# Kernel optimization log

Hardware: AMD Instinct MI355X
Metric: run time of the kernel (lower is better)

Reference implementation:

```python
import jax, jax.numpy as jnp
import numpy as np

MAX_DIST = 32  # unidirectional T5-style bucketing: num_buckets = 33
N_HEAD, D_K, D_V = 8, 64, 64


def setup_inputs() -> dict:
    key = jax.random.key(0)
    ks = jax.random.split(key, 9)
    B, S, D = 4, 2048, 512
    q = jax.random.normal(ks[0], (B, S, D), dtype=jnp.float32)
    k = jax.random.normal(ks[1], (B, S, D), dtype=jnp.float32)
    v = jax.random.normal(ks[2], (B, S, D), dtype=jnp.float32)
    mask = jax.random.randint(ks[3], (B, 1, 1, S), 0, 2, dtype=jnp.int32)
    sc = 1.0 / np.sqrt(D)
    Wq = jax.random.normal(ks[4], (D, D), dtype=jnp.float32) * sc
    Wk = jax.random.normal(ks[5], (D, D), dtype=jnp.float32) * sc
    Wv = jax.random.normal(ks[6], (D, D), dtype=jnp.float32) * sc
    Wfc = jax.random.normal(ks[7], (D, D), dtype=jnp.float32) * sc
    rel_bias = jax.random.normal(ks[8], (MAX_DIST + 1, N_HEAD), dtype=jnp.float32)
    return {"q": q, "k": k, "v": v, "mask": mask, "Wq": Wq, "Wk": Wk,
            "Wv": Wv, "Wfc": Wfc, "rel_bias": rel_bias}


def _rel_pos_bias(rel_bias, seq_len):
    # unidirectional: bucket = clamp(max(context - memory, 0), 0, MAX_DIST)
    pos = jnp.arange(seq_len)
    n = pos[:, None] - pos[None, :]              # context - memory = -relative_position
    bucket = jnp.clip(jnp.maximum(n, 0), 0, MAX_DIST)
    vals = rel_bias[bucket]                      # (S, S, H)
    return jnp.transpose(vals, (2, 0, 1))[None]  # (1, H, S, S)


def reference(q, k, v, mask, Wq, Wk, Wv, Wfc, rel_bias):
    B, Sq, _ = q.shape
    Sk = k.shape[1]
    scale = D_K ** (-0.5)
    qh = (q @ Wq).reshape(B, Sq, N_HEAD, D_K).transpose(0, 2, 1, 3)  # bhsd
    kh = (k @ Wk).reshape(B, Sk, N_HEAD, D_K).transpose(0, 2, 1, 3)
    vh = (v @ Wv).reshape(B, Sk, N_HEAD, D_V).transpose(0, 2, 1, 3)
    attn = jnp.einsum('bhqd,bhkd->bhqk', qh, kh) * scale
    attn = attn + _rel_pos_bias(rel_bias, Sq)
    attn = jnp.where(mask == 0, jnp.float32(-1e9), attn)
    attn = jax.nn.softmax(attn, axis=-1)          # dropout is identity at eval
    out = jnp.einsum('bhqk,bhkd->bhqd', attn, vh)
    out = out.transpose(0, 2, 1, 3).reshape(B, Sq, N_HEAD * D_V)
    out = out @ Wfc
    return out, attn
```

## Files before the change

### kernel.cpp

```cpp
#include <hip/hip_runtime.h>


typedef __attribute__((ext_vector_type(8))) short bfrag;
typedef __attribute__((ext_vector_type(4))) short s16x4;
typedef __attribute__((ext_vector_type(4))) float f32x4;
typedef unsigned int u32;

#define MFMA16(a,b,c) __builtin_amdgcn_mfma_f32_16x16x32_bf16(a,b,c,0,0,0)

__device__ __forceinline__ void gl_lds16(const void* g, void* l){
  __builtin_amdgcn_global_load_lds((const __attribute__((address_space(1))) u32*)g,
                                   (__attribute__((address_space(3))) u32*)l, 16, 0, 0);
}
__device__ __forceinline__ short f2bs(float f){
  u32 u = __float_as_uint(f);
  u = (u + 0x7fffu + ((u>>16)&1u)) >> 16;
  return (short)u;
}
__device__ __forceinline__ float b2f(short s){
  return __uint_as_float(((u32)(unsigned short)s) << 16);
}

#define BB 4
#define HH 8
#define SS 2048
#define DD 512

#define WQT_OFF  0u
#define WKT_OFF  524288u
#define WVT_OFF  1048576u
#define WFCT_OFF 1572864u
#define QB_OFF   2097152u
#define KB_OFF   10485760u
#define VB_OFF   18874368u
#define QH_OFF   27262976u
#define KH_OFF   35651584u
#define VT_OFF   44040192u
#define OH_OFF   52428800u

__global__ __launch_bounds__(256) void conv_w_k(const float* w0,const float* w1,
                                                const float* w2,const float* w3, char* ws){
  const float* w; short* o;
  switch(blockIdx.z){
    case 0:  w=w0; o=(short*)(ws+WQT_OFF); break;
    case 1:  w=w1; o=(short*)(ws+WKT_OFF); break;
    case 2:  w=w2; o=(short*)(ws+WVT_OFF); break;
    default: w=w3; o=(short*)(ws+WFCT_OFF); break;
  }
  int t  = blockIdx.x*256 + threadIdx.x;
  int n  = t >> 6;
  int k0 = (t & 63) << 3;
  bfrag v;
  #pragma unroll
  for (int j=0;j<8;++j) v[j] = f2bs(w[(k0+j)*512 + n]);
  *(bfrag*)(o + n*512 + k0) = v;
}

__global__ __launch_bounds__(256) void conv_x_k(const float* x0,const float* x1,
                                                const float* x2, char* ws){
  const float* x; short* o;
  switch(blockIdx.z){
    case 0:  x=x0; o=(short*)(ws+QB_OFF); break;
    case 1:  x=x1; o=(short*)(ws+KB_OFF); break;
    default: x=x2; o=(short*)(ws+VB_OFF); break;
  }
  int i = (blockIdx.x*256 + threadIdx.x) << 3;
  float4 a = *(const float4*)(x+i);
  float4 b = *(const float4*)(x+i+4);
  bfrag v;
  v[0]=f2bs(a.x); v[1]=f2bs(a.y); v[2]=f2bs(a.z); v[3]=f2bs(a.w);
  v[4]=f2bs(b.x); v[5]=f2bs(b.y); v[6]=f2bs(b.z); v[7]=f2bs(b.w);
  *(bfrag*)(o+i) = v;
}

__device__ void gemm_core(const short* A, const short* Bt, char* Cout, int mode, int bid){
  __shared__ __align__(16) char lds[32768];
  int i0, j0;
  if (mode==1){ i0 = (bid&3)<<7; j0 = (bid>>2)<<7; }
  else        { i0 = (bid>>2)<<7; j0 = (bid&3)<<7; }
  int tid = threadIdx.x;
  int l = tid & 63, w = tid >> 6;
  int wr = (w>>1)<<6, wc = (w&1)<<6;
  int l15 = l & 15, l4 = l >> 4;
  f32x4 acc[4][4];
  #pragma unroll
  for(int a=0;a<4;++a)
    #pragma unroll
    for(int b=0;b<4;++b) acc[a][b] = (f32x4){0.f,0.f,0.f,0.f};
  const char* Ab = (const char*)A;
  const char* Bb = (const char*)Bt;
  for (int kk=0; kk<8; ++kk){
    #pragma unroll
    for (int it=0; it<4; ++it){
      int ci = it*256 + tid;
      int row = ci>>3, cc = ci&7;
      gl_lds16(Ab + (size_t)(i0+row)*1024 + kk*128 + ((cc^(row&7))<<4),
               lds + ((it*256 + w*64)<<4));
      gl_lds16(Bb + (size_t)(j0+row)*1024 + kk*128 + ((cc^(row&7))<<4),
               lds + 16384 + ((it*256 + w*64)<<4));
    }
    asm volatile("s_waitcnt vmcnt(0)" ::: "memory");
    __syncthreads();
    #pragma unroll
    for (int kb=0; kb<2; ++kb){
      bfrag af[4], bf[4];
      #pragma unroll
      for (int mi=0;mi<4;++mi){
        int row = wr + mi*16 + l15;
        af[mi] = *(const bfrag*)(lds + row*128 + (((kb*4 + l4) ^ (row&7))<<4));
      }
      #pragma unroll
      for (int ni=0;ni<4;++ni){
        int row = wc + ni*16 + l15;
        bf[ni] = *(const bfrag*)(lds + 16384 + row*128 + (((kb*4 + l4) ^ (row&7))<<4));
      }
      #pragma unroll
      for (int mi=0;mi<4;++mi)
        #pragma unroll
        for (int ni=0;ni<4;++ni)
          acc[mi][ni] = MFMA16(af[mi], bf[ni], acc[mi][ni]);
    }
    __syncthreads();
  }
  #pragma unroll
  for (int mi=0;mi<4;++mi){
    #pragma unroll
    for (int ni=0;ni<4;++ni){
      #pragma unroll
      for (int r=0;r<4;++r){
        int i = i0 + wr + mi*16 + (l4<<2) + r;
        int j = j0 + wc + ni*16 + l15;
        float v = acc[mi][ni][r];
        if (mode==2){
          ((float*)Cout)[(size_t)i*512 + j] = v;
        } else if (mode==0){
          size_t o = ((size_t)(((i>>11)<<3) + (j>>6))*2048 + (size_t)(i&2047))*64 + (j&63);
          ((short*)Cout)[o] = f2bs(v);
        } else {
          size_t o = ((size_t)(((j>>11)<<3) + (i>>6))*64 + (size_t)(i&63))*2048 + (j&2047);
          ((short*)Cout)[o] = f2bs(v);
        }
      }
    }
  }
}

__global__ __launch_bounds__(256,2) void gemm_proj_k(char* ws){
  switch(blockIdx.z){
    case 0:  gemm_core((const short*)(ws+QB_OFF),  (const short*)(ws+WQT_OFF), ws+QH_OFF, 0, blockIdx.x); break;
    case 1:  gemm_core((const short*)(ws+KB_OFF),  (const short*)(ws+WKT_OFF), ws+KH_OFF, 0, blockIdx.x); break;
    default: gemm_core((const short*)(ws+WVT_OFF), (const short*)(ws+VB_OFF),  ws+VT_OFF, 1, blockIdx.x); break;
  }
}
__global__ __launch_bounds__(256,2) void gemm_final_k(char* ws, float* out){
  gemm_core((const short*)(ws+OH_OFF), (const short*)(ws+WFCT_OFF), (char*)out, 2, blockIdx.x);
}

#define MSK_OFF_L   65536
#define BIAS_OFF_L  73728
#define WSUM_OFF_L  73872
#define RECIP_OFF_L 74384
#define PVRED_OFF_L 74448
#define LDS_TOTAL   78592

__global__ __launch_bounds__(512,1) void attn_k(char* ws, const int* mask,
                                                const float* rel_bias, float* attn_out){
  extern __shared__ __align__(16) char sm[];
  int tid = threadIdx.x;
  int l = tid & 63, w = tid >> 6;
  int l15 = l & 15, l4 = l >> 4;
  int bh = blockIdx.x, qblk = blockIdx.y;
  int b = bh >> 3, h = bh & 7;
  const short* qhb = (const short*)(ws+QH_OFF) + (size_t)bh*SS*64;
  const char*  khb = ws + KH_OFF + (size_t)bh*SS*128;
  const char*  vtb = ws + VT_OFF + (size_t)bh*64*SS*2;

  {
    const int4* m4 = (const int4*)(mask + b*SS);
    int4 ma = m4[tid];
    float4* mf = (float4*)(sm + MSK_OFF_L);
    mf[tid] = make_float4(ma.x?1.f:0.f, ma.y?1.f:0.f, ma.z?1.f:0.f, ma.w?1.f:0.f);
  }
  if (tid < 33) ((float*)(sm+BIAS_OFF_L))[tid] = rel_bias[tid*HH + h];

  int qrow = (qblk<<4) + l15;
  bfrag qA0 = *(const bfrag*)(qhb + (size_t)qrow*64 + l4*8);
  bfrag qA1 = *(const bfrag*)(qhb + (size_t)qrow*64 + 32 + l4*8);
  const float* biasl = (const float*)(sm+BIAS_OFF_L);
  const float* maskl = (const float*)(sm+MSK_OFF_L);
  float rsum[4] = {0.f,0.f,0.f,0.f};

  __syncthreads();

  int wbase = w << 8;
  #pragma unroll 2
  for (int t=0; t<16; ++t){
    int rowk = wbase + (t<<4) + l15;
    const char* kr = khb + (size_t)rowk*128 + (l4<<4);
    bfrag b0 = *(const bfrag*)(kr);
    bfrag b1 = *(const bfrag*)(kr + 64);
    f32x4 acc = (f32x4){0.f,0.f,0.f,0.f};
    acc = MFMA16(qA0, b0, acc);
    acc = MFMA16(qA1, b1, acc);
    float mval = maskl[rowk];
    int rl0 = l4<<2;
    int byte = rowk<<1;
    #pragma unroll
    for (int r=0;r<4;++r){
      int rowl = rl0 + r;
      int n = (qblk<<4) + rowl - rowk;
      n = n<0 ? 0 : (n>32 ? 32 : n);
      float s = acc[r]*0.125f + biasl[n];
      float p = mval * __expf(s);
      rsum[r] += p;
      int ch = (byte>>4) ^ rowl;
      *(short*)(sm + rowl*4096 + (ch<<4) + (byte&15)) = f2bs(p);
    }
  }

  {
    float* wsum = (float*)(sm+WSUM_OFF_L);
    #pragma unroll
    for (int r=0;r<4;++r){
      float s = rsum[r];
      s += __shfl_xor(s,1); s += __shfl_xor(s,2);
      s += __shfl_xor(s,4); s += __shfl_xor(s,8);
      if (l15==0) wsum[(w<<4) + (l4<<2) + r] = s;
    }
  }
  __syncthreads();
  if (tid < 16){
    float* wsum = (float*)(sm+WSUM_OFF_L);
    float t = 0.f;
    #pragma unroll
    for (int i=0;i<8;++i) t += wsum[(i<<4) + tid];
    ((float*)(sm+RECIP_OFF_L))[tid] = 1.f/t;
  }
  __syncthreads();
  const float* recip = (const float*)(sm+RECIP_OFF_L);

  f32x4 acco = (f32x4){0.f,0.f,0.f,0.f};
  int dbase = (w&3)<<4;
  int khalf = w>>2;
  int chbase = khalf<<7;
  const char* vr = vtb + (size_t)(dbase + l15)*4096 + (khalf<<11) + (l4<<4);
  #pragma unroll 4
  for (int vc=0; vc<32; ++vc){
    int ch = (chbase + (vc<<2) + l4) ^ l15;
    bfrag af = *(const bfrag*)(sm + l15*4096 + (ch<<4));
    bfrag bv = *(const bfrag*)(vr + (vc<<6));
    acco = MFMA16(af, bv, acco);
  }
  {
    f32x4* pvred = (f32x4*)(sm+PVRED_OFF_L);
    if (w >= 4) pvred[((w-4)<<6) + l] = acco;
    __syncthreads();
    if (w < 4){
      acco += pvred[(w<<6) + l];
      short* oh = (short*)(ws + OH_OFF);
      #pragma unroll
      for (int r=0;r<4;++r){
        int rowl = (l4<<2) + r;
        float rc = recip[rowl];
        size_t sg = (size_t)b*SS + (qblk<<4) + rowl;
        oh[sg*512 + h*64 + dbase + l15] = f2bs(acco[r]*rc);
      }
    }
  }

  {
    float* dst0 = attn_out + (size_t)bh*SS*SS + (size_t)(qblk<<4)*SS;
    #pragma unroll
    for (int rr=0; rr<2; ++rr){
      int rowl = (w<<1) + rr;
      float rc = recip[rowl];
      float* dst = dst0 + (size_t)rowl*SS;
      #pragma unroll
      for (int it=0; it<8; ++it){
        int col  = it*256 + (l<<2);
        int byte = col<<1;
        int ch = (byte>>4) ^ rowl;
        s16x4 pv = *(const s16x4*)(sm + rowl*4096 + (ch<<4) + (byte&15));
        f32x4 o = (f32x4){b2f(pv[0])*rc, b2f(pv[1])*rc, b2f(pv[2])*rc, b2f(pv[3])*rc};
        __builtin_nontemporal_store(o, (f32x4*)(dst+col));
      }
    }
  }
}

extern "C" void kernel_launch(void* const* d_in, const int* in_sizes, int n_in,
                              void* d_out, int out_size, void* d_ws, size_t ws_size,
                              hipStream_t stream){
  const float* q   = (const float*)d_in[0];
  const float* k   = (const float*)d_in[1];
  const float* v   = (const float*)d_in[2];
  const int*  mask = (const int*)  d_in[3];
  const float* Wq  = (const float*)d_in[4];
  const float* Wk  = (const float*)d_in[5];
  const float* Wv  = (const float*)d_in[6];
  const float* Wfc = (const float*)d_in[7];
  const float* rb  = (const float*)d_in[8];
  char* ws = (char*)d_ws;
  float* out  = (float*)d_out;
  float* attn = out + (size_t)BB*SS*512;

  (void)hipFuncSetAttribute((const void*)attn_k,
        hipFuncAttributeMaxDynamicSharedMemorySize, LDS_TOTAL);

  conv_w_k<<<dim3(128,1,4), 256, 0, stream>>>(Wq, Wk, Wv, Wfc, ws);
  conv_x_k<<<dim3(2048,1,3), 256, 0, stream>>>(q, k, v, ws);
  gemm_proj_k<<<dim3(256,1,3), 256, 0, stream>>>(ws);
  attn_k<<<dim3(32,128), 512, LDS_TOTAL, stream>>>(ws, mask, rb, attn);
  gemm_final_k<<<dim3(256,1,1), 256, 0, stream>>>(ws, out);
}
```

Baseline: 331.7 us.

## Make attention kernel persistent with double-buffered P tiles to overlap attn stores

The attention kernel now launches 256 persistent blocks, each handling 16 consecutive query tiles of one head. It double-buffers the bf16 probability tile in LDS so the previous tile's fp32 attention-matrix stores run interleaved with the next tile's QK^T and softmax work. The per-block mask and bias setup is amortized across tiles, and bias lookup is skipped for key chunks entirely outside the clamp window. LDS use roughly doubles and the kernel adds more barriers, which limits occupancy to one block per CU.

```diff
diff --git a/kernel.cpp b/kernel.cpp
--- a/kernel.cpp
+++ b/kernel.cpp
@@ -7,6 +7,9 @@
 typedef unsigned int u32;
 
 #define MFMA16(a,b,c) __builtin_amdgcn_mfma_f32_16x16x32_bf16(a,b,c,0,0,0)
+
+#define BAR() do{ asm volatile("s_waitcnt lgkmcnt(0)" ::: "memory"); \
+                  __builtin_amdgcn_s_barrier(); }while(0)
 
 __device__ __forceinline__ void gl_lds16(const void* g, void* l){
   __builtin_amdgcn_global_load_lds((const __attribute__((address_space(1))) u32*)g,
@@ -156,12 +159,14 @@
   gemm_core((const short*)(ws+OH_OFF), (const short*)(ws+WFCT_OFF), (char*)out, 2, blockIdx.x);
 }
 
-#define MSK_OFF_L   65536
-#define BIAS_OFF_L  73728
-#define WSUM_OFF_L  73872
-#define RECIP_OFF_L 74384
-#define PVRED_OFF_L 74448
-#define LDS_TOTAL   78592
+#define P0_OFF      0
+#define P1_OFF      65536
+#define MSK_OFF_L   131072
+#define BIAS_OFF_L  139264
+#define WSUM_OFF_L  139424
+#define RECIP_OFF_L 139968
+#define PVRED_OFF_L 140032
+#define LDS_TOTAL   144128
 
 __global__ __launch_bounds__(512,1) void attn_k(char* ws, const int* mask,
                                                 const float* rel_bias, float* attn_out){
@@ -169,11 +174,13 @@
   int tid = threadIdx.x;
   int l = tid & 63, w = tid >> 6;
   int l15 = l & 15, l4 = l >> 4;
-  int bh = blockIdx.x, qblk = blockIdx.y;
+  int j = blockIdx.x;
+  int bh = j & 31, qc = j >> 5;
   int b = bh >> 3, h = bh & 7;
   const short* qhb = (const short*)(ws+QH_OFF) + (size_t)bh*SS*64;
   const char*  khb = ws + KH_OFF + (size_t)bh*SS*128;
   const char*  vtb = ws + VT_OFF + (size_t)bh*64*SS*2;
+  float* attb = attn_out + (size_t)bh*SS*SS;
 
   {
     const int4* m4 = (const int4*)(mask + b*SS);
@@ -182,108 +189,144 @@
     mf[tid] = make_float4(ma.x?1.f:0.f, ma.y?1.f:0.f, ma.z?1.f:0.f, ma.w?1.f:0.f);
   }
   if (tid < 33) ((float*)(sm+BIAS_OFF_L))[tid] = rel_bias[tid*HH + h];
-
-  int qrow = (qblk<<4) + l15;
-  bfrag qA0 = *(const bfrag*)(qhb + (size_t)qrow*64 + l4*8);
-  bfrag qA1 = *(const bfrag*)(qhb + (size_t)qrow*64 + 32 + l4*8);
+  float bias0  = rel_bias[h];
+  float bias32 = rel_bias[32*HH + h];
   const float* biasl = (const float*)(sm+BIAS_OFF_L);
   const float* maskl = (const float*)(sm+MSK_OFF_L);
-  float rsum[4] = {0.f,0.f,0.f,0.f};
-
-  __syncthreads();
-
-  int wbase = w << 8;
-  #pragma unroll 2
-  for (int t=0; t<16; ++t){
-    int rowk = wbase + (t<<4) + l15;
-    const char* kr = khb + (size_t)rowk*128 + (l4<<4);
-    bfrag b0 = *(const bfrag*)(kr);
-    bfrag b1 = *(const bfrag*)(kr + 64);
-    f32x4 acc = (f32x4){0.f,0.f,0.f,0.f};
-    acc = MFMA16(qA0, b0, acc);
-    acc = MFMA16(qA1, b1, acc);
-    float mval = maskl[rowk];
-    int rl0 = l4<<2;
-    int byte = rowk<<1;
-    #pragma unroll
-    for (int r=0;r<4;++r){
-      int rowl = rl0 + r;
-      int n = (qblk<<4) + rowl - rowk;
-      n = n<0 ? 0 : (n>32 ? 32 : n);
-      float s = acc[r]*0.125f + biasl[n];
-      float p = mval * __expf(s);
-      rsum[r] += p;
-      int ch = (byte>>4) ^ rowl;
-      *(short*)(sm + rowl*4096 + (ch<<4) + (byte&15)) = f2bs(p);
-    }
-  }
-
-  {
-    float* wsum = (float*)(sm+WSUM_OFF_L);
-    #pragma unroll
-    for (int r=0;r<4;++r){
-      float s = rsum[r];
-      s += __shfl_xor(s,1); s += __shfl_xor(s,2);
-      s += __shfl_xor(s,4); s += __shfl_xor(s,8);
-      if (l15==0) wsum[(w<<4) + (l4<<2) + r] = s;
-    }
-  }
-  __syncthreads();
-  if (tid < 16){
-    float* wsum = (float*)(sm+WSUM_OFF_L);
-    float t = 0.f;
-    #pragma unroll
-    for (int i=0;i<8;++i) t += wsum[(i<<4) + tid];
-    ((float*)(sm+RECIP_OFF_L))[tid] = 1.f/t;
-  }
-  __syncthreads();
   const float* recip = (const float*)(sm+RECIP_OFF_L);
-
-  f32x4 acco = (f32x4){0.f,0.f,0.f,0.f};
-  int dbase = (w&3)<<4;
-  int khalf = w>>2;
-  int chbase = khalf<<7;
-  const char* vr = vtb + (size_t)(dbase + l15)*4096 + (khalf<<11) + (l4<<4);
-  #pragma unroll 4
-  for (int vc=0; vc<32; ++vc){
-    int ch = (chbase + (vc<<2) + l4) ^ l15;
-    bfrag af = *(const bfrag*)(sm + l15*4096 + (ch<<4));
-    bfrag bv = *(const bfrag*)(vr + (vc<<6));
-    acco = MFMA16(af, bv, acco);
-  }
-  {
-    f32x4* pvred = (f32x4*)(sm+PVRED_OFF_L);
-    if (w >= 4) pvred[((w-4)<<6) + l] = acco;
-    __syncthreads();
-    if (w < 4){
-      acco += pvred[(w<<6) + l];
-      short* oh = (short*)(ws + OH_OFF);
-      #pragma unroll
-      for (int r=0;r<4;++r){
-        int rowl = (l4<<2) + r;
-        float rc = recip[rowl];
-        size_t sg = (size_t)b*SS + (qblk<<4) + rowl;
-        oh[sg*512 + h*64 + dbase + l15] = f2bs(acco[r]*rc);
-      }
-    }
-  }
-
-  {
-    float* dst0 = attn_out + (size_t)bh*SS*SS + (size_t)(qblk<<4)*SS;
-    #pragma unroll
-    for (int rr=0; rr<2; ++rr){
-      int rowl = (w<<1) + rr;
-      float rc = recip[rowl];
-      float* dst = dst0 + (size_t)rowl*SS;
-      #pragma unroll
-      for (int it=0; it<8; ++it){
-        int col  = it*256 + (l<<2);
+  int rl0 = l4<<2;
+  int qprev = 0;
+
+  for (int item=0; item<16; ++item){
+    int qblk = (qc<<4) + item;
+    char* pcur = sm + ((item&1) ? P1_OFF : P0_OFF);
+    const char* pprv = sm + ((item&1) ? P0_OFF : P1_OFF);
+
+    BAR();
+
+    float rcA = recip[(w<<1)];
+    float rcB = recip[(w<<1)+1];
+    float* dstp = attb + (size_t)(qprev<<4)*SS;
+
+    int qrow = (qblk<<4) + l15;
+    bfrag qA0 = *(const bfrag*)(qhb + (size_t)qrow*64 + l4*8);
+    bfrag qA1 = *(const bfrag*)(qhb + (size_t)qrow*64 + 32 + l4*8);
+    float rsum[4] = {0.f,0.f,0.f,0.f};
+    int r0 = qblk<<4;
+
+    #pragma unroll 2
+    for (int t=0; t<16; ++t){
+      int c0 = (w<<8) + (t<<4);
+      int rowk = c0 + l15;
+      const char* kr = khb + (size_t)rowk*128 + (l4<<4);
+      bfrag b0 = *(const bfrag*)(kr);
+      bfrag b1 = *(const bfrag*)(kr + 64);
+      if (item > 0){
+        int rowl = (w<<1) + (t>>3);
+        int col  = ((t&7)<<8) + (l<<2);
         int byte = col<<1;
         int ch = (byte>>4) ^ rowl;
-        s16x4 pv = *(const s16x4*)(sm + rowl*4096 + (ch<<4) + (byte&15));
+        s16x4 pv = *(const s16x4*)(pprv + rowl*4096 + (ch<<4) + (byte&15));
+        float rc = (t>>3) ? rcB : rcA;
         f32x4 o = (f32x4){b2f(pv[0])*rc, b2f(pv[1])*rc, b2f(pv[2])*rc, b2f(pv[3])*rc};
-        __builtin_nontemporal_store(o, (f32x4*)(dst+col));
-      }
+        __builtin_nontemporal_store(o, (f32x4*)(dstp + (size_t)rowl*SS + col));
+      }
+      f32x4 acc = (f32x4){0.f,0.f,0.f,0.f};
+      acc = MFMA16(qA0, b0, acc);
+      acc = MFMA16(qA1, b1, acc);
+      float mval = maskl[rowk];
+      float pr[4];
+      if (c0 >= r0+16){
+        #pragma unroll
+        for (int r=0;r<4;++r) pr[r] = __expf(acc[r]*0.125f + bias0);
+      } else if (c0 <= r0-47){
+        #pragma unroll
+        for (int r=0;r<4;++r) pr[r] = __expf(acc[r]*0.125f + bias32);
+      } else {
+        #pragma unroll
+        for (int r=0;r<4;++r){
+          int n = r0 + rl0 + r - rowk;
+          n = n<0 ? 0 : (n>32 ? 32 : n);
+          pr[r] = __expf(acc[r]*0.125f + biasl[n]);
+        }
+      }
+      int byte = rowk<<1;
+      #pragma unroll
+      for (int r=0;r<4;++r){
+        float p = mval * pr[r];
+        rsum[r] += p;
+        int rowl = rl0 + r;
+        int ch = (byte>>4) ^ rowl;
+        *(short*)(pcur + rowl*4096 + (ch<<4) + (byte&15)) = f2bs(p);
+      }
+    }
+
+    {
+      float* wsum = (float*)(sm+WSUM_OFF_L);
+      #pragma unroll
+      for (int r=0;r<4;++r){
+        float s = rsum[r];
+        s += __shfl_xor(s,1); s += __shfl_xor(s,2);
+        s += __shfl_xor(s,4); s += __shfl_xor(s,8);
+        if (l15==0) wsum[(w<<4) + rl0 + r] = s;
+      }
+    }
+    BAR();
+    if (tid < 16){
+      float* wsum = (float*)(sm+WSUM_OFF_L);
+      float t2 = 0.f;
+      #pragma unroll
+      for (int i=0;i<8;++i) t2 += wsum[(i<<4) + tid];
+      ((float*)(sm+RECIP_OFF_L))[tid] = 1.f/t2;
+    }
+    BAR();
+
+    f32x4 acco = (f32x4){0.f,0.f,0.f,0.f};
+    int dbase = (w&3)<<4;
+    int khalf = w>>2;
+    int chbase = khalf<<7;
+    const char* vr = vtb + (size_t)(dbase + l15)*4096 + (khalf<<11) + (l4<<4);
+    #pragma unroll 4
+    for (int vc=0; vc<32; ++vc){
+      int ch = (chbase + (vc<<2) + l4) ^ l15;
+      bfrag af = *(const bfrag*)(pcur + l15*4096 + (ch<<4));
+      bfrag bv = *(const bfrag*)(vr + (vc<<6));
+      acco = MFMA16(af, bv, acco);
+    }
+    {
+      f32x4* pvred = (f32x4*)(sm+PVRED_OFF_L);
+      if (w >= 4) pvred[((w-4)<<6) + l] = acco;
+      BAR();
+      if (w < 4){
+        acco += pvred[(w<<6) + l];
+        short* oh = (short*)(ws + OH_OFF);
+        #pragma unroll
+        for (int r=0;r<4;++r){
+          int rowl = rl0 + r;
+          float rc = recip[rowl];
+          size_t sg = (size_t)b*SS + (qblk<<4) + rowl;
+          oh[sg*512 + h*64 + dbase + l15] = f2bs(acco[r]*rc);
+        }
+      }
+    }
+    qprev = qblk;
+  }
+
+  {
+    const char* plast = sm + P1_OFF;
+    float* dstp = attb + (size_t)(qprev<<4)*SS;
+    float rcA = recip[(w<<1)];
+    float rcB = recip[(w<<1)+1];
+    #pragma unroll
+    for (int t=0; t<16; ++t){
+      int rowl = (w<<1) + (t>>3);
+      int col  = ((t&7)<<8) + (l<<2);
+      int byte = col<<1;
+      int ch = (byte>>4) ^ rowl;
+      s16x4 pv = *(const s16x4*)(plast + rowl*4096 + (ch<<4) + (byte&15));
+      float rc = (t>>3) ? rcB : rcA;
+      f32x4 o = (f32x4){b2f(pv[0])*rc, b2f(pv[1])*rc, b2f(pv[2])*rc, b2f(pv[3])*rc};
+      __builtin_nontemporal_store(o, (f32x4*)(dstp + (size_t)rowl*SS + col));
     }
   }
 }
@@ -310,6 +353,6 @@
   conv_w_k<<<dim3(128,1,4), 256, 0, stream>>>(Wq, Wk, Wv, Wfc, ws);
   conv_x_k<<<dim3(2048,1,3), 256, 0, stream>>>(q, k, v, ws);
   gemm_proj_k<<<dim3(256,1,3), 256, 0, stream>>>(ws);
-  attn_k<<<dim3(32,128), 512, LDS_TOTAL, stream>>>(ws, mask, rb, attn);
+  attn_k<<<dim3(256), 512, LDS_TOTAL, stream>>>(ws, mask, rb, attn);
   gemm_final_k<<<dim3(256,1,1), 256, 0, stream>>>(ws, out);
 }
```

Result: slower. 391.0 us (+17.9%).

## Recompute QK scores in fp32 for attn output and swap MFMA operand order

Applied to the files above, without the earlier changes.

The attention kernel swaps the MFMA A/B operands so each lane holds four consecutive key columns for one query row. That lets mask loads, bf16 packing and LDS stores become vector operations, and the row sum needs only two shuffles. Bias lookup is skipped for tiles entirely outside the bucketing window. The fp32 attention output is now written by recomputing QK^T and exp in a second pass and scaling by the reciprocal, instead of reading back bf16 probabilities from LDS. This trades extra MFMA, exp work and K reloads for higher precision and fewer LDS reads, and it also raises launch-bounds occupancy and replaces syncthreads with a custom barrier.

```diff
diff --git a/kernel.cpp b/kernel.cpp
--- a/kernel.cpp
+++ b/kernel.cpp
@@ -1,12 +1,15 @@
 #include <hip/hip_runtime.h>
+#include <hip/hip_bf16.h>
 
 
 typedef __attribute__((ext_vector_type(8))) short bfrag;
-typedef __attribute__((ext_vector_type(4))) short s16x4;
 typedef __attribute__((ext_vector_type(4))) float f32x4;
 typedef unsigned int u32;
 
 #define MFMA16(a,b,c) __builtin_amdgcn_mfma_f32_16x16x32_bf16(a,b,c,0,0,0)
+
+#define BAR() do{ asm volatile("s_waitcnt lgkmcnt(0)" ::: "memory"); \
+                  __builtin_amdgcn_s_barrier(); }while(0)
 
 __device__ __forceinline__ void gl_lds16(const void* g, void* l){
   __builtin_amdgcn_global_load_lds((const __attribute__((address_space(1))) u32*)g,
@@ -17,8 +20,10 @@
   u = (u + 0x7fffu + ((u>>16)&1u)) >> 16;
   return (short)u;
 }
-__device__ __forceinline__ float b2f(short s){
-  return __uint_as_float(((u32)(unsigned short)s) << 16);
+__device__ __forceinline__ u32 pack2(float a, float b){
+  float2 t; t.x = a; t.y = b;
+  __hip_bfloat162 h = __float22bfloat162_rn(t);
+  return *(u32*)&h;
 }
 
 #define BB 4
@@ -163,7 +168,7 @@
 #define PVRED_OFF_L 74448
 #define LDS_TOTAL   78592
 
-__global__ __launch_bounds__(512,1) void attn_k(char* ws, const int* mask,
+__global__ __launch_bounds__(512,4) void attn_k(char* ws, const int* mask,
                                                 const float* rel_bias, float* attn_out){
   extern __shared__ __align__(16) char sm[];
   int tid = threadIdx.x;
@@ -182,62 +187,104 @@
     mf[tid] = make_float4(ma.x?1.f:0.f, ma.y?1.f:0.f, ma.z?1.f:0.f, ma.w?1.f:0.f);
   }
   if (tid < 33) ((float*)(sm+BIAS_OFF_L))[tid] = rel_bias[tid*HH + h];
+  float bias0  = rel_bias[h];
+  float bias32 = rel_bias[32*HH + h];
+  const float* biasl = (const float*)(sm+BIAS_OFF_L);
+  const float* maskl = (const float*)(sm+MSK_OFF_L);
 
   int qrow = (qblk<<4) + l15;
   bfrag qA0 = *(const bfrag*)(qhb + (size_t)qrow*64 + l4*8);
   bfrag qA1 = *(const bfrag*)(qhb + (size_t)qrow*64 + 32 + l4*8);
-  const float* biasl = (const float*)(sm+BIAS_OFF_L);
-  const float* maskl = (const float*)(sm+MSK_OFF_L);
-  float rsum[4] = {0.f,0.f,0.f,0.f};
+  int r0 = qblk<<4;
+  int wbase = w << 8;
 
   __syncthreads();
 
-  int wbase = w << 8;
+  float rs = 0.f;
   #pragma unroll 2
   for (int t=0; t<16; ++t){
-    int rowk = wbase + (t<<4) + l15;
-    const char* kr = khb + (size_t)rowk*128 + (l4<<4);
+    int c0 = wbase + (t<<4);
+    const char* kr = khb + (size_t)(c0 + l15)*128 + (l4<<4);
     bfrag b0 = *(const bfrag*)(kr);
     bfrag b1 = *(const bfrag*)(kr + 64);
     f32x4 acc = (f32x4){0.f,0.f,0.f,0.f};
-    acc = MFMA16(qA0, b0, acc);
-    acc = MFMA16(qA1, b1, acc);
-    float mval = maskl[rowk];
-    int rl0 = l4<<2;
-    int byte = rowk<<1;
-    #pragma unroll
-    for (int r=0;r<4;++r){
-      int rowl = rl0 + r;
-      int n = (qblk<<4) + rowl - rowk;
-      n = n<0 ? 0 : (n>32 ? 32 : n);
-      float s = acc[r]*0.125f + biasl[n];
-      float p = mval * __expf(s);
-      rsum[r] += p;
-      int ch = (byte>>4) ^ rowl;
-      *(short*)(sm + rowl*4096 + (ch<<4) + (byte&15)) = f2bs(p);
-    }
+    acc = MFMA16(b0, qA0, acc);
+    acc = MFMA16(b1, qA1, acc);
+    float4 m4v = *(const float4*)(maskl + c0 + (l4<<2));
+    float pr[4];
+    if (c0 >= r0+16){
+      #pragma unroll
+      for (int r=0;r<4;++r) pr[r] = __expf(acc[r]*0.125f + bias0);
+    } else if (c0 <= r0-47){
+      #pragma unroll
+      for (int r=0;r<4;++r) pr[r] = __expf(acc[r]*0.125f + bias32);
+    } else {
+      #pragma unroll
+      for (int r=0;r<4;++r){
+        int n = (r0 + l15) - (c0 + (l4<<2) + r);
+        n = n<0 ? 0 : (n>32 ? 32 : n);
+        pr[r] = __expf(acc[r]*0.125f + biasl[n]);
+      }
+    }
+    float p0 = m4v.x*pr[0], p1 = m4v.y*pr[1], p2 = m4v.z*pr[2], p3 = m4v.w*pr[3];
+    rs += (p0+p1)+(p2+p3);
+    int byte = (c0 + (l4<<2)) << 1;
+    int ch = (byte>>4) ^ l15;
+    uint2 pk; pk.x = pack2(p0,p1); pk.y = pack2(p2,p3);
+    *(uint2*)(sm + l15*4096 + (ch<<4) + (byte&15)) = pk;
   }
 
   {
+    rs += __shfl_xor(rs, 16);
+    rs += __shfl_xor(rs, 32);
     float* wsum = (float*)(sm+WSUM_OFF_L);
-    #pragma unroll
-    for (int r=0;r<4;++r){
-      float s = rsum[r];
-      s += __shfl_xor(s,1); s += __shfl_xor(s,2);
-      s += __shfl_xor(s,4); s += __shfl_xor(s,8);
-      if (l15==0) wsum[(w<<4) + (l4<<2) + r] = s;
-    }
-  }
-  __syncthreads();
+    if (l < 16) wsum[(w<<4) + l15] = rs;
+  }
+  BAR();
   if (tid < 16){
     float* wsum = (float*)(sm+WSUM_OFF_L);
-    float t = 0.f;
-    #pragma unroll
-    for (int i=0;i<8;++i) t += wsum[(i<<4) + tid];
-    ((float*)(sm+RECIP_OFF_L))[tid] = 1.f/t;
-  }
-  __syncthreads();
+    float t2 = 0.f;
+    #pragma unroll
+    for (int i=0;i<8;++i) t2 += wsum[(i<<4) + tid];
+    ((float*)(sm+RECIP_OFF_L))[tid] = 1.f/t2;
+  }
+  BAR();
   const float* recip = (const float*)(sm+RECIP_OFF_L);
+
+  {
+    float rc = recip[l15];
+    float* dst = attn_out + (size_t)bh*SS*SS + (size_t)(r0 + l15)*SS
+               + wbase + (l4<<2);
+    #pragma unroll 4
+    for (int t=0; t<16; ++t){
+      int c0 = wbase + (t<<4);
+      const char* kr = khb + (size_t)(c0 + l15)*128 + (l4<<4);
+      bfrag b0 = *(const bfrag*)(kr);
+      bfrag b1 = *(const bfrag*)(kr + 64);
+      f32x4 acc = (f32x4){0.f,0.f,0.f,0.f};
+      acc = MFMA16(b0, qA0, acc);
+      acc = MFMA16(b1, qA1, acc);
+      float4 m4v = *(const float4*)(maskl + c0 + (l4<<2));
+      float pr[4];
+      if (c0 >= r0+16){
+        #pragma unroll
+        for (int r=0;r<4;++r) pr[r] = __expf(acc[r]*0.125f + bias0);
+      } else if (c0 <= r0-47){
+        #pragma unroll
+        for (int r=0;r<4;++r) pr[r] = __expf(acc[r]*0.125f + bias32);
+      } else {
+        #pragma unroll
+        for (int r=0;r<4;++r){
+          int n = (r0 + l15) - (c0 + (l4<<2) + r);
+          n = n<0 ? 0 : (n>32 ? 32 : n);
+          pr[r] = __expf(acc[r]*0.125f + biasl[n]);
+        }
+      }
+      f32x4 o = (f32x4){ m4v.x*pr[0]*rc, m4v.y*pr[1]*rc,
+                         m4v.z*pr[2]*rc, m4v.w*pr[3]*rc };
+      *(f32x4*)(dst + (t<<4)) = o;
+    }
+  }
 
   f32x4 acco = (f32x4){0.f,0.f,0.f,0.f};
   int dbase = (w&3)<<4;
@@ -254,7 +301,7 @@
   {
     f32x4* pvred = (f32x4*)(sm+PVRED_OFF_L);
     if (w >= 4) pvred[((w-4)<<6) + l] = acco;
-    __syncthreads();
+    BAR();
     if (w < 4){
       acco += pvred[(w<<6) + l];
       short* oh = (short*)(ws + OH_OFF);
@@ -264,25 +311,6 @@
         float rc = recip[rowl];
         size_t sg = (size_t)b*SS + (qblk<<4) + rowl;
         oh[sg*512 + h*64 + dbase + l15] = f2bs(acco[r]*rc);
-      }
-    }
-  }
-
-  {
-    float* dst0 = attn_out + (size_t)bh*SS*SS + (size_t)(qblk<<4)*SS;
-    #pragma unroll
-    for (int rr=0; rr<2; ++rr){
-      int rowl = (w<<1) + rr;
-      float rc = recip[rowl];
-      float* dst = dst0 + (size_t)rowl*SS;
-      #pragma unroll
-      for (int it=0; it<8; ++it){
-        int col  = it*256 + (l<<2);
-        int byte = col<<1;
-        int ch = (byte>>4) ^ rowl;
-        s16x4 pv = *(const s16x4*)(sm + rowl*4096 + (ch<<4) + (byte&15));
-        f32x4 o = (f32x4){b2f(pv[0])*rc, b2f(pv[1])*rc, b2f(pv[2])*rc, b2f(pv[3])*rc};
-        __builtin_nontemporal_store(o, (f32x4*)(dst+col));
       }
     }
   }
```

Result: slower. 451.1 us (+36.0%).
